# Performance work log

Hardware: AMD Instinct MI355X
Metric: run time of the kernel (lower is better)

## Reference

```python
import jax, jax.numpy as jnp
import numpy as np


def setup_inputs() -> dict:
    key = jax.random.key(0)
    k1, k2 = jax.random.split(key)
    B, T, D = 16, 512, 384
    x = jax.random.normal(k1, (B, T, D), dtype=jnp.float32)
    durations = jax.random.randint(k2, (B, T), 0, 8, dtype=jnp.int64)
    return {"x": x, "durations": durations, "max_len": 4096}


def reference(x, durations, max_len):
    # x: [B, T, D], durations: [B, T] int, max_len: static int
    # Each phoneme t is repeated durations[b, t] times along the frame axis,
    # then sequences are zero-padded to a common length.
    cum = jnp.cumsum(durations, axis=1)              # [B, T] exclusive upper bounds
    frames = jnp.arange(max_len)                     # [F]
    # frame f belongs to phoneme idx where cum[idx-1] <= f < cum[idx]
    idx = jax.vmap(lambda c: jnp.searchsorted(c, frames, side="right"))(cum)  # [B, F]
    valid = frames[None, :] < cum[:, -1][:, None]    # [B, F] frames past total -> pad
    idx = jnp.minimum(idx, durations.shape[1] - 1)   # clamp out-of-range gather
    out = jnp.take_along_axis(x, idx[:, :, None], axis=1)  # [B, F, D]
    return jnp.where(valid[:, :, None], out, jnp.zeros((), dtype=x.dtype))
```

## Files before the change

kernel.cpp:

```cpp
#include <hip/hip_runtime.h>

#define BB 16
#define TT 512
#define FF 4096
#define DD 384
#define DD4 (DD / 4)
#define FPB 8

__global__ __launch_bounds__(TT) void build_idx_kernel(
    const int* __restrict__ dur, int* __restrict__ fidx) {
    const int b = blockIdx.x;
    const int t = threadIdx.x;
    int* fb = fidx + b * FF;

#pragma unroll
    for (int k = 0; k < FF / TT; ++k) fb[k * TT + t] = -1;

    __shared__ int s[TT];
    const int d = dur[b * TT + t];
    s[t] = d;
    __syncthreads();
#pragma unroll
    for (int off = 1; off < TT; off <<= 1) {
        int v = (t >= off) ? s[t - off] : 0;
        __syncthreads();
        s[t] += v;
        __syncthreads();
    }
    const int cum = s[t];
    const int start = cum - d;
    const int end = cum < FF ? cum : FF;
    for (int f = start; f < end; ++f) fb[f] = t;
}

__global__ __launch_bounds__(256) void gather_kernel(
    const float4* __restrict__ x, const int* __restrict__ fidx,
    float4* __restrict__ out) {
    const int tilesPerBatch = FF / FPB;
    const int bid = blockIdx.x;
    const int b = bid / tilesPerBatch;
    const int tile = bid - b * tilesPerBatch;
    const int f0 = tile * FPB;

    __shared__ int idx8[FPB];
    if (threadIdx.x < FPB)
        idx8[threadIdx.x] = fidx[b * FF + f0 + threadIdx.x];
    __syncthreads();

    const float4* xb = x + (size_t)b * TT * DD4;
    float4* ob = out + ((size_t)b * FF + f0) * DD4;

#pragma unroll
    for (int k = 0; k < 3; ++k) {
        const int pos = k * 256 + (int)threadIdx.x;
        const int fl = pos / DD4;
        const int c = pos - fl * DD4;
        const int idx = idx8[fl];
        float4 v;
        if (idx >= 0) {
            v = xb[(size_t)idx * DD4 + c];
        } else {
            v = make_float4(0.f, 0.f, 0.f, 0.f);
        }
        ob[pos] = v;
    }
}

extern "C" void kernel_launch(void* const* d_in, const int* in_sizes, int n_in,
                              void* d_out, int out_size, void* d_ws, size_t ws_size,
                              hipStream_t stream) {
    const float* x = (const float*)d_in[0];
    const int* dur = (const int*)d_in[1];
    int* fidx = (int*)d_ws;

    build_idx_kernel<<<BB, TT, 0, stream>>>(dur, fidx);
    gather_kernel<<<BB * (FF / FPB), 256, 0, stream>>>(
        (const float4*)x, fidx, (float4*)d_out);
}
```

Measured before the change: 120.1 us.

## Fuse index build and gather into one kernel with per-tile prefix scan

Merges the cumsum/index-building kernel and the gather kernel into one launch. Each block of 512 threads recomputes the full 512-element duration prefix scan in shared memory and fills a 32-frame index table locally, then gathers 32 frames of rows. This removes the second launch and the global index workspace round trip, but every one of the 2048 blocks now repeats the scan with its nine barrier rounds.

```diff
diff --git a/kernel.cpp b/kernel.cpp
--- a/kernel.cpp
+++ b/kernel.cpp
@@ -1,24 +1,28 @@
 #include <hip/hip_runtime.h>
 
-#define BB 16
-#define TT 512
-#define FF 4096
-#define DD 384
-#define DD4 (DD / 4)
-#define FPB 8
+#define BB   16
+#define TT   512
+#define FF   4096
+#define DD4  96
+#define FPT  32
+#define TILES (FF / FPT)
+#define NTHR 512
 
-__global__ __launch_bounds__(TT) void build_idx_kernel(
-    const int* __restrict__ dur, int* __restrict__ fidx) {
-    const int b = blockIdx.x;
-    const int t = threadIdx.x;
-    int* fb = fidx + b * FF;
-
-#pragma unroll
-    for (int k = 0; k < FF / TT; ++k) fb[k * TT + t] = -1;
+__global__ __launch_bounds__(NTHR) void lenreg_fused_kernel(
+    const float4* __restrict__ x, const int* __restrict__ dur,
+    float4* __restrict__ out) {
+    const int bid  = blockIdx.x;
+    const int b    = bid / TILES;
+    const int tile = bid - b * TILES;
+    const int f0   = tile * FPT;
+    const int t    = threadIdx.x;
 
     __shared__ int s[TT];
+    __shared__ int sidx[FPT];
+
     const int d = dur[b * TT + t];
     s[t] = d;
+    if (t < FPT) sidx[t] = -1;
     __syncthreads();
 #pragma unroll
     for (int off = 1; off < TT; off <<= 1) {
@@ -27,53 +31,37 @@
         s[t] += v;
         __syncthreads();
     }
-    const int cum = s[t];
+
+    const int cum   = s[t];
     const int start = cum - d;
-    const int end = cum < FF ? cum : FF;
-    for (int f = start; f < end; ++f) fb[f] = t;
-}
-
-__global__ __launch_bounds__(256) void gather_kernel(
-    const float4* __restrict__ x, const int* __restrict__ fidx,
-    float4* __restrict__ out) {
-    const int tilesPerBatch = FF / FPB;
-    const int bid = blockIdx.x;
-    const int b = bid / tilesPerBatch;
-    const int tile = bid - b * tilesPerBatch;
-    const int f0 = tile * FPB;
-
-    __shared__ int idx8[FPB];
-    if (threadIdx.x < FPB)
-        idx8[threadIdx.x] = fidx[b * FF + f0 + threadIdx.x];
+    int lo = start > f0 ? start : f0;
+    int hi = cum < f0 + FPT ? cum : f0 + FPT;
+    for (int f = lo; f < hi; ++f) sidx[f - f0] = t;
     __syncthreads();
 
     const float4* xb = x + (size_t)b * TT * DD4;
     float4* ob = out + ((size_t)b * FF + f0) * DD4;
-
 #pragma unroll
-    for (int k = 0; k < 3; ++k) {
-        const int pos = k * 256 + (int)threadIdx.x;
-        const int fl = pos / DD4;
-        const int c = pos - fl * DD4;
-        const int idx = idx8[fl];
-        float4 v;
+    for (int k = 0; k < (FPT * DD4) / NTHR; ++k) {
+        const int pos = k * NTHR + t;
+        const int fl  = pos / DD4;
+        const int c   = pos - fl * DD4;
+        const int idx = sidx[fl];
+        float4 vv;
         if (idx >= 0) {
-            v = xb[(size_t)idx * DD4 + c];
+            vv = xb[(size_t)idx * DD4 + c];
         } else {
-            v = make_float4(0.f, 0.f, 0.f, 0.f);
+            vv = make_float4(0.f, 0.f, 0.f, 0.f);
         }
-        ob[pos] = v;
+        ob[pos] = vv;
     }
 }
 
 extern "C" void kernel_launch(void* const* d_in, const int* in_sizes, int n_in,
                               void* d_out, int out_size, void* d_ws, size_t ws_size,
                               hipStream_t stream) {
-    const float* x = (const float*)d_in[0];
-    const int* dur = (const int*)d_in[1];
-    int* fidx = (int*)d_ws;
-
-    build_idx_kernel<<<BB, TT, 0, stream>>>(dur, fidx);
-    gather_kernel<<<BB * (FF / FPB), 256, 0, stream>>>(
-        (const float4*)x, fidx, (float4*)d_out);
+    const float* x  = (const float*)d_in[0];
+    const int* dur  = (const int*)d_in[1];
+    lenreg_fused_kernel<<<BB * TILES, NTHR, 0, stream>>>(
+        (const float4*)x, dur, (float4*)d_out);
 }
```

New measurement: 121.4 us. No clear change (+1.1%).
